# Performance work log

Measured on AMD Instinct MI355X. Metric: run time of the kernel, lower is better.

The kernel has to match this reference:

```python
import jax, jax.numpy as jnp
import numpy as np

D_MODEL = 1024


def setup_inputs() -> dict:
    key = jax.random.key(0)
    k1, k2, k3, k4, k5, k6 = jax.random.split(key, 6)
    B, S, D = 4, 4096, D_MODEL
    scale = 1.0 / np.sqrt(D)
    return {
        "hidden": jax.random.normal(k1, (B, S, D), dtype=jnp.float32),
        "pre_emb": jax.random.normal(k2, (B, S, D), dtype=jnp.float32),
        "w1": jax.random.normal(k3, (D, D), dtype=jnp.float32) * scale,  # [in, out]
        "b1": jax.random.normal(k4, (D,), dtype=jnp.float32) * 0.01,
        "w2": jax.random.normal(k5, (D, D), dtype=jnp.float32) * scale,
        "b2": jax.random.normal(k6, (D,), dtype=jnp.float32) * 0.01,
    }


def reference(hidden, pre_emb, w1, b1, w2, b2):
    # h = Linear1(hidden); i = Linear2(hidden + pre_emb)
    h = jnp.einsum("bsd,de->bse", hidden, w1) + b1            # [B,S,D]
    i = jnp.einsum("bsd,de->bse", hidden + pre_emb, w2) + b2  # [B,S,D]
    attn = jnp.einsum("bqd,bkd->bqk", h, i)                   # [B,S,S]
    return jax.nn.softmax(attn, axis=-1)
```

## Files before the change

### kernel.cpp

```cpp
#include <hip/hip_runtime.h>
#include <hip/hip_bf16.h>
#include <stdint.h>

#define DM   1024
#define BATCH 4
#define SEQ  4096
#define MTOT (BATCH*SEQ)

typedef __attribute__((ext_vector_type(8))) short bf16x8;
typedef __attribute__((ext_vector_type(4))) float f32x4;

#define GLOAD_LDS16(gp, lp) __builtin_amdgcn_global_load_lds( \
    (const __attribute__((address_space(1))) unsigned int*)(gp), \
    (__attribute__((address_space(3))) unsigned int*)(lp), 16, 0, 0)

#define VMCNT(n) asm volatile("s_waitcnt vmcnt(" #n ")" ::: "memory")
#define BAR()    __builtin_amdgcn_s_barrier()
#define FENCE()  asm volatile("" ::: "memory")

__device__ __forceinline__ ushort f2bf(float f){
  uint u = __float_as_uint(f);
  u += 0x7FFFu + ((u >> 16) & 1u);
  return (ushort)(u >> 16);
}
__device__ __forceinline__ float bf2f(ushort b){ return __uint_as_float(((uint)b) << 16); }

__device__ __forceinline__ void split4(const float4 v, ushort4& h4, ushort4& l4){
  h4.x = f2bf(v.x); l4.x = f2bf(v.x - bf2f(h4.x));
  h4.y = f2bf(v.y); l4.y = f2bf(v.y - bf2f(h4.y));
  h4.z = f2bf(v.z); l4.z = f2bf(v.z - bf2f(h4.z));
  h4.w = f2bf(v.w); l4.w = f2bf(v.w - bf2f(h4.w));
}

__global__ __launch_bounds__(256)
void prep_w_split(const float* __restrict__ w1, const float* __restrict__ w2,
                  ushort* __restrict__ w1h, ushort* __restrict__ w1l,
                  ushort* __restrict__ w2h, ushort* __restrict__ w2l){
  const float* w = blockIdx.y ? w2 : w1;
  ushort* oh = blockIdx.y ? w2h : w1h;
  ushort* ol = blockIdx.y ? w2l : w1l;
  size_t off = ((size_t)blockIdx.x * 256 + threadIdx.x) * 4;
  float4 v = *(const float4*)&w[off];
  ushort4 h4, l4; split4(v, h4, l4);
  *(ushort4*)&oh[off] = h4;
  *(ushort4*)&ol[off] = l4;
}

__global__ __launch_bounds__(256)
void prep_xy(const float* __restrict__ hidden, const float* __restrict__ pre,
             ushort* __restrict__ xh, ushort* __restrict__ xl,
             ushort* __restrict__ yh, ushort* __restrict__ yl,
             const float* __restrict__ c2, float* __restrict__ beta, int writeX){
  __shared__ float red[4];
  const int tid = threadIdx.x, lane = tid & 63, wid = tid >> 6;
  size_t off = ((size_t)blockIdx.x * 256 + tid) * 4;
  float4 h = *(const float4*)&hidden[off];
  float4 p = *(const float4*)&pre[off];
  float4 y = {h.x + p.x, h.y + p.y, h.z + p.z, h.w + p.w};
  ushort4 a, b;
  if (writeX){
    split4(h, a, b);
    *(ushort4*)&xh[off] = a;
    *(ushort4*)&xl[off] = b;
  }
  split4(y, a, b);
  *(ushort4*)&yh[off] = a;
  *(ushort4*)&yl[off] = b;

  float4 c = *(const float4*)&c2[tid * 4];
  float s = y.x * c.x + y.y * c.y + y.z * c.z + y.w * c.w;
  #pragma unroll
  for (int o = 32; o > 0; o >>= 1) s += __shfl_xor(s, o, 64);
  if (lane == 0) red[wid] = s;
  __syncthreads();
  if (tid == 0) beta[blockIdx.x] = red[0] + red[1] + red[2] + red[3];
}

__global__ __launch_bounds__(256)
void c2k(const float* __restrict__ w2, const float* __restrict__ b1,
         float* __restrict__ c2){
  const int wid = threadIdx.x >> 6, lane = threadIdx.x & 63;
  const int row = blockIdx.x * 4 + wid;
  float s = 0.f;
  #pragma unroll
  for (int t = 0; t < 16; t++){
    int e = lane + 64 * t;
    s += w2[(size_t)row * DM + e] * b1[e];
  }
  #pragma unroll
  for (int o = 32; o > 0; o >>= 1) s += __shfl_xor(s, o, 64);
  if (lane == 0) c2[row] = s;
}

__device__ __forceinline__ void mainloop256(
    const ushort* __restrict__ Aph, const ushort* __restrict__ Apl,
    const ushort* __restrict__ Bph, const ushort* __restrict__ Bpl,
    int m0, int n0, f32x4 (&acc)[8][4]){
  __shared__ alignas(16) ushort lds[2][4][256*32];

  const int tid = threadIdx.x;
  const int lane = tid & 63, wv = tid >> 6;
  const int wm = (wv & 1) * 128, wn = (wv >> 1) * 64;
  const int lr = lane & 15;
  const int lks = (((lane >> 4) ^ ((lane >> 1) & 3)) << 3);

  const int rowidx = tid >> 2;
  const int srcc = (((tid & 3) ^ ((tid >> 3) & 3)) << 3);
  const int arow = rowidx + (rowidx & 64);
  const int brow = ((rowidx >> 5) << 6) + (rowidx & 31);
  const int awrow = wv * 16 + ((wv & 4) << 4);
  const int bwrow = ((wv >> 1) << 6) + ((wv & 1) << 4);

  auto stageA = [&](int bf, int qa, int kt){
    const size_t g = (size_t)(m0 + qa * 64 + arow) * DM + kt * 32 + srcc;
    GLOAD_LDS16(Aph + g, &lds[bf][0][(qa * 64 + awrow) * 32]);
    GLOAD_LDS16(Apl + g, &lds[bf][1][(qa * 64 + awrow) * 32]);
  };
  auto stageB = [&](int bf, int qb, int kt){
    const size_t g = (size_t)(n0 + qb * 32 + brow) * DM + kt * 32 + srcc;
    GLOAD_LDS16(Bph + g, &lds[bf][2][(qb * 32 + bwrow) * 32]);
    GLOAD_LDS16(Bpl + g, &lds[bf][3][(qb * 32 + bwrow) * 32]);
  };

  bf16x8 ah[4], al[4], bh0[2], bl0[2], bh1[2], bl1[2];

#define DS_A(CUR, QA) do { _Pragma("unroll") for (int i = 0; i < 4; i++){ \
    ah[i] = *(const bf16x8*)&lds[CUR][0][(wm + (QA)*64 + i*16 + lr)*32 + lks]; \
    al[i] = *(const bf16x8*)&lds[CUR][1][(wm + (QA)*64 + i*16 + lr)*32 + lks]; } } while(0)
#define DS_B(CUR, QB, BH, BL) do { _Pragma("unroll") for (int j = 0; j < 2; j++){ \
    BH[j] = *(const bf16x8*)&lds[CUR][2][(wn + (QB)*32 + j*16 + lr)*32 + lks]; \
    BL[j] = *(const bf16x8*)&lds[CUR][3][(wn + (QB)*32 + j*16 + lr)*32 + lks]; } } while(0)
#define MFMA3(QA, QB, BH, BL) do { \
  __builtin_amdgcn_s_setprio(1); \
  _Pragma("unroll") for (int i = 0; i < 4; i++) _Pragma("unroll") for (int j = 0; j < 2; j++) \
    acc[(QA)*4+i][(QB)*2+j] = __builtin_amdgcn_mfma_f32_16x16x32_bf16(ah[i], BH[j], acc[(QA)*4+i][(QB)*2+j], 0, 0, 0); \
  _Pragma("unroll") for (int i = 0; i < 4; i++) _Pragma("unroll") for (int j = 0; j < 2; j++) \
    acc[(QA)*4+i][(QB)*2+j] = __builtin_amdgcn_mfma_f32_16x16x32_bf16(ah[i], BL[j], acc[(QA)*4+i][(QB)*2+j], 0, 0, 0); \
  _Pragma("unroll") for (int i = 0; i < 4; i++) _Pragma("unroll") for (int j = 0; j < 2; j++) \
    acc[(QA)*4+i][(QB)*2+j] = __builtin_amdgcn_mfma_f32_16x16x32_bf16(al[i], BH[j], acc[(QA)*4+i][(QB)*2+j], 0, 0, 0); \
  __builtin_amdgcn_s_setprio(0); } while(0)

  stageA(0, 0, 0); stageB(0, 0, 0); stageB(0, 1, 0); stageA(0, 1, 0);

  for (int t = 0; t < 31; ++t){
    const int cur = t & 1, nxt = cur ^ 1;
    VMCNT(4); BAR(); FENCE();
    DS_A(cur, 0); DS_B(cur, 0, bh0, bl0);
    stageA(nxt, 0, t + 1);
    MFMA3(0, 0, bh0, bl0);
    BAR();
    VMCNT(4); BAR(); FENCE();
    DS_B(cur, 1, bh1, bl1);
    stageB(nxt, 0, t + 1);
    MFMA3(0, 1, bh1, bl1);
    BAR();
    VMCNT(4); BAR(); FENCE();
    DS_A(cur, 1);
    stageB(nxt, 1, t + 1);
    MFMA3(1, 1, bh1, bl1);
    BAR();
    stageA(nxt, 1, t + 1);
    MFMA3(1, 0, bh0, bl0);
    BAR();
  }
  {
    VMCNT(4); BAR(); FENCE();
    DS_A(1, 0); DS_B(1, 0, bh0, bl0);
    MFMA3(0, 0, bh0, bl0);
    BAR();
    VMCNT(2); BAR(); FENCE();
    DS_B(1, 1, bh1, bl1);
    MFMA3(0, 1, bh1, bl1);
    BAR();
    VMCNT(0); BAR(); FENCE();
    DS_A(1, 1);
    MFMA3(1, 1, bh1, bl1);
    BAR();
    MFMA3(1, 0, bh0, bl0);
  }
#undef DS_A
#undef DS_B
#undef MFMA3
}

__global__ __launch_bounds__(512, 2)
void gemm_bt_split256(const ushort* __restrict__ Aph, const ushort* __restrict__ Apl,
                      const ushort* __restrict__ Bph, const ushort* __restrict__ Bpl,
                      ushort* __restrict__ oh, ushort* __restrict__ ol){
  const int m0 = blockIdx.y * 256, n0 = blockIdx.x * 256;
  f32x4 acc[8][4] = {};
  mainloop256(Aph, Apl, Bph, Bpl, m0, n0, acc);

  const int tid = threadIdx.x, lane = tid & 63, wv = tid >> 6;
  const int wm = (wv & 1) * 128, wn = (wv >> 1) * 64;
  const int lr = lane & 15, rbase = (lane >> 4) * 4;
  #pragma unroll
  for (int I = 0; I < 8; I++)
    #pragma unroll
    for (int J = 0; J < 4; J++){
      int gc = n0 + wn + J*16 + lr;
      #pragma unroll
      for (int r = 0; r < 4; r++){
        int gr = m0 + wm + I*16 + rbase + r;
        float v = acc[I][J][r];
        ushort hb = f2bf(v);
        size_t o = (size_t)gr * DM + gc;
        oh[o] = hb;
        ol[o] = f2bf(v - bf2f(hb));
      }
    }
}

__global__ __launch_bounds__(512, 2)
void gemm_bt_f32_256(const ushort* __restrict__ Aph, const ushort* __restrict__ Apl,
                     const ushort* __restrict__ Bph, const ushort* __restrict__ Bpl,
                     float* __restrict__ out){
  const int b = blockIdx.y;
  const int id = blockIdx.x;
  const int c = id & 7;
  const int m = id >> 3;
  const int qt = (c >> 1) * 4 + (m >> 3);
  const int kt = (c & 1) * 8 + (m & 7);
  const int m0 = qt * 256, n0 = kt * 256;
  const size_t abase = (size_t)b * SEQ * DM;

  f32x4 acc[8][4] = {};
  mainloop256(Aph + abase, Apl + abase, Bph + abase, Bpl + abase, m0, n0, acc);

  const int tid = threadIdx.x, lane = tid & 63, wv = tid >> 6;
  const int wm = (wv & 1) * 128, wn = (wv >> 1) * 64;
  const int lr = lane & 15, rbase = (lane >> 4) * 4;
  #pragma unroll
  for (int I = 0; I < 8; I++)
    #pragma unroll
    for (int J = 0; J < 4; J++){
      int gc = n0 + wn + J*16 + lr;
      #pragma unroll
      for (int r = 0; r < 4; r++){
        int gr = m0 + wm + I*16 + rbase + r;
        __builtin_nontemporal_store(acc[I][J][r],
            &out[((size_t)b * SEQ + gr) * SEQ + gc]);
      }
    }
}

__device__ __forceinline__ void bt_mainloop(
    const ushort* __restrict__ Aph, const ushort* __restrict__ Apl,
    const ushort* __restrict__ Bph, const ushort* __restrict__ Bpl,
    int m0, int n0, f32x4 (&acc)[4][4]){
  __shared__ alignas(16) ushort Ah[128*32];
  __shared__ alignas(16) ushort Al[128*32];
  __shared__ alignas(16) ushort Bh[128*32];
  __shared__ alignas(16) ushort Bl[128*32];

  const int tid = threadIdx.x;
  const int lane = tid & 63, wid = tid >> 6;
  const int wm = (wid & 1) * 64, wn = (wid >> 1) * 64;
  const int lr = lane & 15;
  const int lks = (((lane >> 4) ^ ((lane >> 1) & 3)) << 3);

  const ushort* plane = (wid == 0) ? Aph : (wid == 1) ? Apl : (wid == 2) ? Bph : Bpl;
  ushort* lds = (wid == 0) ? Ah : (wid == 1) ? Al : (wid == 2) ? Bh : Bl;
  const int r0 = (wid < 2) ? m0 : n0;
  const size_t goff = (size_t)(r0 + (lane >> 2)) * DM
                    + (size_t)(((lane & 3) ^ ((lane >> 3) & 3)) * 8);

  for (int k0 = 0; k0 < DM; k0 += 32){
    __syncthreads();
    const ushort* gp = plane + goff + k0;
    #pragma unroll
    for (int t = 0; t < 8; t++){
      GLOAD_LDS16(gp + (size_t)t * 16 * DM, lds + t * 512);
    }
    __syncthreads();

    bf16x8 fah[4], fal[4], fbh[4], fbl[4];
    #pragma unroll
    for (int i = 0; i < 4; i++){
      fah[i] = *(const bf16x8*)&Ah[(wm + i*16 + lr)*32 + lks];
      fal[i] = *(const bf16x8*)&Al[(wm + i*16 + lr)*32 + lks];
      fbh[i] = *(const bf16x8*)&Bh[(wn + i*16 + lr)*32 + lks];
      fbl[i] = *(const bf16x8*)&Bl[(wn + i*16 + lr)*32 + lks];
    }
    #pragma unroll
    for (int i = 0; i < 4; i++)
      #pragma unroll
      for (int j = 0; j < 4; j++){
        acc[i][j] = __builtin_amdgcn_mfma_f32_16x16x32_bf16(fah[i], fbh[j], acc[i][j], 0, 0, 0);
        acc[i][j] = __builtin_amdgcn_mfma_f32_16x16x32_bf16(fah[i], fbl[j], acc[i][j], 0, 0, 0);
        acc[i][j] = __builtin_amdgcn_mfma_f32_16x16x32_bf16(fal[i], fbh[j], acc[i][j], 0, 0, 0);
      }
  }
}

__global__ __launch_bounds__(256, 2)
void gemm_bt_split(const ushort* __restrict__ Aph, const ushort* __restrict__ Apl,
                   const ushort* __restrict__ Bph, const ushort* __restrict__ Bpl,
                   ushort* __restrict__ oh, ushort* __restrict__ ol){
  const int m0 = blockIdx.y * 128, n0 = blockIdx.x * 128;
  f32x4 acc[4][4];
  for (int i = 0; i < 4; i++) for (int j = 0; j < 4; j++) acc[i][j] = (f32x4){0.f,0.f,0.f,0.f};
  bt_mainloop(Aph, Apl, Bph, Bpl, m0, n0, acc);

  const int lane = threadIdx.x & 63, wid = threadIdx.x >> 6;
  const int wm = (wid & 1) * 64, wn = (wid >> 1) * 64;
  const int lr = lane & 15;
  const int rbase = (lane >> 4) * 4;
  #pragma unroll
  for (int i = 0; i < 4; i++)
    #pragma unroll
    for (int j = 0; j < 4; j++){
      int gc = n0 + wn + j*16 + lr;
      #pragma unroll
      for (int r = 0; r < 4; r++){
        int gr = m0 + wm + i*16 + rbase + r;
        float v = acc[i][j][r];
        ushort hb = f2bf(v);
        size_t o = (size_t)gr * DM + gc;
        oh[o] = hb;
        ol[o] = f2bf(v - bf2f(hb));
      }
    }
}

#define ASTR 40
__global__ __launch_bounds__(256, 2)
void gemm_z_manual(const float* __restrict__ hidden,
                   const ushort* __restrict__ gth, const ushort* __restrict__ gtl,
                   ushort* __restrict__ zh, ushort* __restrict__ zl){
  const int m0 = blockIdx.y * 128, n0 = blockIdx.x * 128;
  __shared__ alignas(16) ushort Ah[128*ASTR];
  __shared__ alignas(16) ushort Al[128*ASTR];
  __shared__ alignas(16) ushort Bh[128*32];
  __shared__ alignas(16) ushort Bl[128*32];

  const int tid = threadIdx.x;
  const int lane = tid & 63, wid = tid >> 6;
  const int wm = (wid & 1) * 64, wn = (wid >> 1) * 64;
  const int lr = lane & 15, lk = (lane >> 4) * 8;
  const int lks = (((lane >> 4) ^ ((lane >> 1) & 3)) << 3);

  const ushort* bp = (wid < 2) ? gth : gtl;
  ushort* blds = (wid < 2) ? Bh : Bl;
  const int tb = (wid & 1) * 4;
  const size_t bgoff = (size_t)(n0 + (lane >> 2)) * DM
                     + (size_t)(((lane & 3) ^ ((lane >> 3) & 3)) * 8);

  f32x4 acc[4][4];
  for (int i = 0; i < 4; i++) for (int j = 0; j < 4; j++) acc[i][j] = (f32x4){0.f,0.f,0.f,0.f};

  for (int k0 = 0; k0 < DM; k0 += 32){
    __syncthreads();
    const ushort* gb = bp + bgoff + k0;
    #pragma unroll
    for (int t = 0; t < 4; t++){
      GLOAD_LDS16(gb + (size_t)(tb + t) * 16 * DM, blds + (tb + t) * 512);
    }
    #pragma unroll
    for (int c = 0; c < 4; c++){
      int idx = c * 256 + tid;
      int row = idx >> 3, kq = (idx & 7) * 4;
      size_t ga = (size_t)(m0 + row) * DM + k0 + kq;
      float4 v = *(const float4*)&hidden[ga];
      ushort4 h4, l4;
      split4(v, h4, l4);
      *(ushort4*)&Ah[row*ASTR + kq] = h4;
      *(ushort4*)&Al[row*ASTR + kq] = l4;
    }
    __syncthreads();

    bf16x8 fah[4], fal[4], fbh[4], fbl[4];
    #pragma unroll
    for (int i = 0; i < 4; i++){
      fah[i] = *(const bf16x8*)&Ah[(wm + i*16 + lr)*ASTR + lk];
      fal[i] = *(const bf16x8*)&Al[(wm + i*16 + lr)*ASTR + lk];
      fbh[i] = *(const bf16x8*)&Bh[(wn + i*16 + lr)*32 + lks];
      fbl[i] = *(const bf16x8*)&Bl[(wn + i*16 + lr)*32 + lks];
    }
    #pragma unroll
    for (int i = 0; i < 4; i++)
      #pragma unroll
      for (int j = 0; j < 4; j++){
        acc[i][j] = __builtin_amdgcn_mfma_f32_16x16x32_bf16(fah[i], fbh[j], acc[i][j], 0, 0, 0);
        acc[i][j] = __builtin_amdgcn_mfma_f32_16x16x32_bf16(fah[i], fbl[j], acc[i][j], 0, 0, 0);
        acc[i][j] = __builtin_amdgcn_mfma_f32_16x16x32_bf16(fal[i], fbh[j], acc[i][j], 0, 0, 0);
      }
  }

  const int rbase = (lane >> 4) * 4;
  #pragma unroll
  for (int i = 0; i < 4; i++)
    #pragma unroll
    for (int j = 0; j < 4; j++){
      int gc = n0 + wn + j*16 + lr;
      #pragma unroll
      for (int r = 0; r < 4; r++){
        int gr = m0 + wm + i*16 + rbase + r;
        float v = acc[i][j][r];
        ushort hb = f2bf(v);
        size_t o = (size_t)gr * DM + gc;
        zh[o] = hb;
        zl[o] = f2bf(v - bf2f(hb));
      }
    }
}

__global__ __launch_bounds__(256)
void softmax_rows(float* __restrict__ out, const float* __restrict__ beta){
  __shared__ float red[8];
  const size_t row = blockIdx.x;
  float* p = out + row * (size_t)SEQ;
  const float* bp = beta + ((row >> 12) << 12);
  const int tid = threadIdx.x, lane = tid & 63, wid = tid >> 6;

  f32x4 v[4];
  float m = -3.0e38f;
  #pragma unroll
  for (int c = 0; c < 4; c++){
    v[c] = __builtin_nontemporal_load(((const f32x4*)p) + c*256 + tid);
    f32x4 bb = *(((const f32x4*)bp) + c*256 + tid);
    v[c] += bb;
    m = fmaxf(m, fmaxf(fmaxf(v[c].x, v[c].y), fmaxf(v[c].z, v[c].w)));
  }
  #pragma unroll
  for (int o = 32; o > 0; o >>= 1) m = fmaxf(m, __shfl_xor(m, o, 64));
  if (lane == 0) red[wid] = m;
  __syncthreads();
  const float M = fmaxf(fmaxf(red[0], red[1]), fmaxf(red[2], red[3]));

  float s = 0.f;
  #pragma unroll
  for (int c = 0; c < 4; c++){
    v[c].x = __expf(v[c].x - M); s += v[c].x;
    v[c].y = __expf(v[c].y - M); s += v[c].y;
    v[c].z = __expf(v[c].z - M); s += v[c].z;
    v[c].w = __expf(v[c].w - M); s += v[c].w;
  }
  #pragma unroll
  for (int o = 32; o > 0; o >>= 1) s += __shfl_xor(s, o, 64);
  if (lane == 0) red[4 + wid] = s;
  __syncthreads();
  const float inv = 1.0f / (red[4] + red[5] + red[6] + red[7]);
  #pragma unroll
  for (int c = 0; c < 4; c++){
    v[c] *= inv;
    __builtin_nontemporal_store(v[c], ((f32x4*)p) + c*256 + tid);
  }
}

extern "C" void kernel_launch(void* const* d_in, const int* in_sizes, int n_in,
                              void* d_out, int out_size, void* d_ws, size_t ws_size,
                              hipStream_t stream){
  const float* hidden = (const float*)d_in[0];
  const float* pre    = (const float*)d_in[1];
  const float* w1     = (const float*)d_in[2];
  const float* b1     = (const float*)d_in[3];
  const float* w2     = (const float*)d_in[4];
  float* out = (float*)d_out;

  char* ws = (char*)d_ws;
  const size_t WP = (size_t)DM * DM * sizeof(ushort);
  const size_t AP = (size_t)MTOT * DM * sizeof(ushort);
  const bool big = ws_size >= 6*AP + 6*WP + (1u << 20);

  ushort *w1h, *w1l, *w2h, *w2l, *Gth, *Gtl, *Xh, *Xl, *Yh, *Yl, *Zh, *Zl;
  float *c2, *beta;
  if (big){
    Xh  = (ushort*)(ws + 0*AP);  Xl  = (ushort*)(ws + 1*AP);
    Yh  = (ushort*)(ws + 2*AP);  Yl  = (ushort*)(ws + 3*AP);
    Zh  = (ushort*)(ws + 4*AP);  Zl  = (ushort*)(ws + 5*AP);
    w1h = (ushort*)(ws + 6*AP);          w1l = (ushort*)(ws + 6*AP + WP);
    w2h = (ushort*)(ws + 6*AP + 2*WP);   w2l = (ushort*)(ws + 6*AP + 3*WP);
    Gth = (ushort*)(ws + 6*AP + 4*WP);   Gtl = (ushort*)(ws + 6*AP + 5*WP);
    c2   = (float*)(ws + 6*AP + 6*WP);
    beta = c2 + DM;
  } else {
    Zh  = (ushort*)(ws + 0*AP);  Zl  = (ushort*)(ws + 1*AP);
    Yh  = (ushort*)(ws + 2*AP);  Yl  = (ushort*)(ws + 3*AP);
    Gth = (ushort*)(ws + 4*AP);  Gtl = (ushort*)(ws + 4*AP + WP);
    w1h = (ushort*)(ws + 0);       w1l = (ushort*)(ws + WP);
    w2h = (ushort*)(ws + 2*WP);    w2l = (ushort*)(ws + 3*WP);
    c2   = (float*)(ws + 4*AP + 2*WP);
    beta = c2 + DM;
    Xh = Xl = nullptr;
  }

  prep_w_split<<<dim3(1024, 2), 256, 0, stream>>>(w1, w2, w1h, w1l, w2h, w2l);
  c2k<<<dim3(256), 256, 0, stream>>>(w2, b1, c2);
  prep_xy<<<dim3(16384), 256, 0, stream>>>(hidden, pre, Xh, Xl, Yh, Yl, c2, beta, big ? 1 : 0);
  gemm_bt_split<<<dim3(8, 8), 256, 0, stream>>>(w2h, w2l, w1h, w1l, Gth, Gtl);
  if (big){
    gemm_bt_split256<<<dim3(4, 64), 512, 0, stream>>>(Xh, Xl, Gth, Gtl, Zh, Zl);
  } else {
    gemm_z_manual<<<dim3(8, 128), 256, 0, stream>>>(hidden, Gth, Gtl, Zh, Zl);
  }
  gemm_bt_f32_256<<<dim3(256, BATCH), 512, 0, stream>>>(Zh, Zl, Yh, Yl, out);
  softmax_rows<<<dim3(MTOT), 256, 0, stream>>>(out, beta);
}
```

Baseline: 866.5 us.

## Collapse GEMM mainloop into two barrier phases with earlier prefetch issue

Restructures the double-buffered bf16 split-precision GEMM mainloop. Each k-step drops from four barrier-separated quarter phases (eight barriers) to two phases (two barriers). Each phase issues its global-to-LDS prefetches for the next tile first, then does larger batched LDS reads and MFMA groups. MFMA priority raising now spans two MFMA groups instead of one. This cuts barrier stalls and lengthens MFMA bursts, at the cost of more register pressure from holding both B fragments, and vmcnt accounting that now depends on the new load ordering.

```diff
diff --git a/kernel.cpp b/kernel.cpp
--- a/kernel.cpp
+++ b/kernel.cpp
@@ -131,52 +131,46 @@
     BH[j] = *(const bf16x8*)&lds[CUR][2][(wn + (QB)*32 + j*16 + lr)*32 + lks]; \
     BL[j] = *(const bf16x8*)&lds[CUR][3][(wn + (QB)*32 + j*16 + lr)*32 + lks]; } } while(0)
 #define MFMA3(QA, QB, BH, BL) do { \
-  __builtin_amdgcn_s_setprio(1); \
   _Pragma("unroll") for (int i = 0; i < 4; i++) _Pragma("unroll") for (int j = 0; j < 2; j++) \
     acc[(QA)*4+i][(QB)*2+j] = __builtin_amdgcn_mfma_f32_16x16x32_bf16(ah[i], BH[j], acc[(QA)*4+i][(QB)*2+j], 0, 0, 0); \
   _Pragma("unroll") for (int i = 0; i < 4; i++) _Pragma("unroll") for (int j = 0; j < 2; j++) \
     acc[(QA)*4+i][(QB)*2+j] = __builtin_amdgcn_mfma_f32_16x16x32_bf16(ah[i], BL[j], acc[(QA)*4+i][(QB)*2+j], 0, 0, 0); \
   _Pragma("unroll") for (int i = 0; i < 4; i++) _Pragma("unroll") for (int j = 0; j < 2; j++) \
     acc[(QA)*4+i][(QB)*2+j] = __builtin_amdgcn_mfma_f32_16x16x32_bf16(al[i], BH[j], acc[(QA)*4+i][(QB)*2+j], 0, 0, 0); \
-  __builtin_amdgcn_s_setprio(0); } while(0)
+  } while(0)
 
   stageA(0, 0, 0); stageB(0, 0, 0); stageB(0, 1, 0); stageA(0, 1, 0);
 
   for (int t = 0; t < 31; ++t){
     const int cur = t & 1, nxt = cur ^ 1;
+    VMCNT(2); BAR(); FENCE();
+    stageA(nxt, 0, t + 1); stageB(nxt, 0, t + 1);
+    DS_A(cur, 0); DS_B(cur, 0, bh0, bl0); DS_B(cur, 1, bh1, bl1);
+    __builtin_amdgcn_s_setprio(1);
+    MFMA3(0, 0, bh0, bl0);
+    MFMA3(0, 1, bh1, bl1);
+    __builtin_amdgcn_s_setprio(0);
     VMCNT(4); BAR(); FENCE();
-    DS_A(cur, 0); DS_B(cur, 0, bh0, bl0);
-    stageA(nxt, 0, t + 1);
+    stageB(nxt, 1, t + 1); stageA(nxt, 1, t + 1);
+    DS_A(cur, 1);
+    __builtin_amdgcn_s_setprio(1);
+    MFMA3(1, 1, bh1, bl1);
+    MFMA3(1, 0, bh0, bl0);
+    __builtin_amdgcn_s_setprio(0);
+  }
+  {
+    VMCNT(2); BAR(); FENCE();
+    DS_A(1, 0); DS_B(1, 0, bh0, bl0); DS_B(1, 1, bh1, bl1);
+    __builtin_amdgcn_s_setprio(1);
     MFMA3(0, 0, bh0, bl0);
-    BAR();
-    VMCNT(4); BAR(); FENCE();
-    DS_B(cur, 1, bh1, bl1);
-    stageB(nxt, 0, t + 1);
     MFMA3(0, 1, bh1, bl1);
-    BAR();
-    VMCNT(4); BAR(); FENCE();
-    DS_A(cur, 1);
-    stageB(nxt, 1, t + 1);
-    MFMA3(1, 1, bh1, bl1);
-    BAR();
-    stageA(nxt, 1, t + 1);
-    MFMA3(1, 0, bh0, bl0);
-    BAR();
-  }
-  {
-    VMCNT(4); BAR(); FENCE();
-    DS_A(1, 0); DS_B(1, 0, bh0, bl0);
-    MFMA3(0, 0, bh0, bl0);
-    BAR();
-    VMCNT(2); BAR(); FENCE();
-    DS_B(1, 1, bh1, bl1);
-    MFMA3(0, 1, bh1, bl1);
-    BAR();
+    __builtin_amdgcn_s_setprio(0);
     VMCNT(0); BAR(); FENCE();
     DS_A(1, 1);
+    __builtin_amdgcn_s_setprio(1);
     MFMA3(1, 1, bh1, bl1);
-    BAR();
     MFMA3(1, 0, bh0, bl0);
+    __builtin_amdgcn_s_setprio(0);
   }
 #undef DS_A
 #undef DS_B
```

Measured after the change: 884.4 us. 1.02x slower.
